# Kernel tuning notes

Measured on AMD Instinct MI355X. Metric: run time of the kernel, lower is better.

Reference implementation:

```python
import jax, jax.numpy as jnp
import numpy as np

# Dims: batch B, seq L, embed D, router hidden H, num_blocks NB, top_k K
B, L, D, H, NB, K = 8, 4096, 1024, 64, 16, 2
TEMP = 2.0          # current_temperature buffer (init 2.0), clamp(min=0.1) inert
LN_EPS = 1e-5


def setup_inputs() -> dict:
    key = jax.random.key(0)
    k_x, k_w1, k_w2 = jax.random.split(key, 3)
    return {
        "x": jax.random.normal(k_x, (B, L, D), dtype=jnp.float32),
        "ln_gamma": jnp.ones((D,), dtype=jnp.float32),
        "ln_beta": jnp.zeros((D,), dtype=jnp.float32),
        "W1": jax.random.normal(k_w1, (D, H), dtype=jnp.float32) / np.sqrt(D).astype(np.float32),
        "W2": jax.random.normal(k_w2, (H, NB), dtype=jnp.float32) / np.sqrt(H).astype(np.float32),
    }


def reference(x, ln_gamma, ln_beta, W1, W2):
    # gate: LayerNorm -> Linear(no bias) -> GELU(exact) -> Linear(no bias)
    mu = jnp.mean(x, axis=-1, keepdims=True)
    var = jnp.mean(jnp.square(x - mu), axis=-1, keepdims=True)
    xn = (x - mu) * jax.lax.rsqrt(var + LN_EPS) * ln_gamma + ln_beta
    h = jax.nn.gelu(xn @ W1, approximate=False)          # (B, L, H)
    logits = (h @ W2) / TEMP                              # (B, L, NB)

    probs = jax.nn.softmax(logits, axis=-1)               # (B, L, NB)
    top_probs, indices = jax.lax.top_k(probs, K)          # (B, L, K) each
    weights = top_probs / (jnp.sum(top_probs, axis=-1, keepdims=True) + 1e-8)

    # load-balancing aux loss: f = fraction of assignments per block (detached),
    # P = mean router prob per block
    counts = jnp.zeros((NB,), dtype=probs.dtype).at[indices.reshape(-1)].add(1.0)
    f = jax.lax.stop_gradient(counts) / (B * L * K + 1e-8)
    P = jnp.mean(probs, axis=(0, 1))                      # (NB,)
    aux_loss = NB * jnp.sum(f * P)

    return probs, indices, aux_loss, weights
```

## Files before the change

kernel.cpp:

```cpp
#include <hip/hip_runtime.h>
#include <math.h>

typedef __attribute__((ext_vector_type(8))) short short8;
typedef __attribute__((ext_vector_type(4))) float f32x4;

#define NTOK 32768
#define DDIM 1024
#define HDIM 64
#define NB 16
#define LN_EPS 1e-5f

#define IDX_OFF ((size_t)NTOK * NB)
#define AUX_OFF (IDX_OFF + (size_t)NTOK * 2)
#define WT_OFF  (AUX_OFF + 1)

#define CS_F   64
#define BP_F   4352
#define PART_F 102656

__device__ __forceinline__ short8 as_s8(uint4 u) {
    union { uint4 u; short8 s; } x; x.u = u; return x.s;
}

__device__ __forceinline__ f32x4 ntload4(const float* p) {
    return __builtin_nontemporal_load((const f32x4*)p);
}

__global__ void pack_kernel(const float* __restrict__ W1,
                            const float* __restrict__ gamma,
                            const float* __restrict__ beta,
                            float* __restrict__ ws) {
    __shared__ float sg[4][64];
    __shared__ float sb[4][64];
    const int s = blockIdx.x;
    const int t = threadIdx.x;

    {
        const int j = t & 63, p = t >> 6;
        float ag = 0.f, ab = 0.f;
        for (int kk = 0; kk < 8; ++kk) {
            const int k = s * 32 + p * 8 + kk;
            const float w = W1[k * HDIM + j];
            ag += gamma[k] * w;
            ab += beta[k] * w;
        }
        sg[p][j] = ag;
        sb[p][j] = ab;
    }

    {
        unsigned int* bp = (unsigned int*)(ws + BP_F);
        const int n = t >> 6;
        const int l = t & 63;
        const int q = l >> 4, c = l & 15;
        const int col = n * 16 + c;
        unsigned int uh[8], um[8], ul[8];
#pragma unroll
        for (int j = 0; j < 8; ++j) {
            const int k = s * 32 + q * 8 + j;
            const float w = gamma[k] * W1[k * HDIM + col];
            const unsigned int hb = __float_as_uint(w) & 0xFFFF0000u;
            const float r = w - __uint_as_float(hb);
            const unsigned int mb = __float_as_uint(r) & 0xFFFF0000u;
            const float r2 = r - __uint_as_float(mb);
            const unsigned int lb = __float_as_uint(r2) & 0xFFFF0000u;
            uh[j] = hb >> 16; um[j] = mb >> 16; ul[j] = lb >> 16;
        }
        const int base = ((s * 4 + n) * 64 + l) * 4;
#pragma unroll
        for (int d = 0; d < 4; ++d) {
            bp[base + d]         = uh[2 * d] | (uh[2 * d + 1] << 16);
            bp[32768 + base + d] = um[2 * d] | (um[2 * d + 1] << 16);
            bp[65536 + base + d] = ul[2 * d] | (ul[2 * d + 1] << 16);
        }
    }
    __syncthreads();
    if (t < 64) {
        atomicAdd(&ws[CS_F + t],      sg[0][t] + sg[1][t] + sg[2][t] + sg[3][t]);
        atomicAdd(&ws[CS_F + 64 + t], sb[0][t] + sb[1][t] + sb[2][t] + sb[3][t]);
    }
}

__device__ __forceinline__ void split8(const f32x4 a0, const f32x4 a1,
                                       short8& AH, short8& AM, short8& AL,
                                       float& s1, float& s2) {
    const float v[8] = {a0.x, a0.y, a0.z, a0.w, a1.x, a1.y, a1.z, a1.w};
    unsigned int ph[4], pm[4], pl[4];
#pragma unroll
    for (int d = 0; d < 4; ++d) {
        const float v0 = v[2 * d], v1 = v[2 * d + 1];
        const unsigned int h0 = __float_as_uint(v0) & 0xFFFF0000u;
        const unsigned int h1 = __float_as_uint(v1) & 0xFFFF0000u;
        const float r0 = v0 - __uint_as_float(h0);
        const float r1 = v1 - __uint_as_float(h1);
        const unsigned int m0 = __float_as_uint(r0) & 0xFFFF0000u;
        const unsigned int m1 = __float_as_uint(r1) & 0xFFFF0000u;
        const float q0 = r0 - __uint_as_float(m0);
        const float q1 = r1 - __uint_as_float(m1);
        ph[d] = (h0 >> 16) | h1;
        pm[d] = (m0 >> 16) | m1;
        pl[d] = (__float_as_uint(q0) >> 16) | (__float_as_uint(q1) & 0xFFFF0000u);
        s1 += v0 + v1;
        s2 = fmaf(v0, v0, fmaf(v1, v1, s2));
    }
    AH = as_s8(make_uint4(ph[0], ph[1], ph[2], ph[3]));
    AM = as_s8(make_uint4(pm[0], pm[1], pm[2], pm[3]));
    AL = as_s8(make_uint4(pl[0], pl[1], pl[2], pl[3]));
}

#define MFMA6(ACC, AH, AM, AL, BH, BM, BL)                                        \
    ACC = __builtin_amdgcn_mfma_f32_16x16x32_bf16(AH, as_s8(BH), ACC, 0, 0, 0);   \
    ACC = __builtin_amdgcn_mfma_f32_16x16x32_bf16(AH, as_s8(BM), ACC, 0, 0, 0);   \
    ACC = __builtin_amdgcn_mfma_f32_16x16x32_bf16(AM, as_s8(BH), ACC, 0, 0, 0);   \
    ACC = __builtin_amdgcn_mfma_f32_16x16x32_bf16(AH, as_s8(BL), ACC, 0, 0, 0);   \
    ACC = __builtin_amdgcn_mfma_f32_16x16x32_bf16(AM, as_s8(BM), ACC, 0, 0, 0);   \
    ACC = __builtin_amdgcn_mfma_f32_16x16x32_bf16(AL, as_s8(BH), ACC, 0, 0, 0);

__global__ __launch_bounds__(256, 2)
void router_main(const float* __restrict__ x,
                 const float* __restrict__ ws_ro,
                 const unsigned int* __restrict__ bp,
                 const float* __restrict__ W2,
                 float* __restrict__ part,
                 float* __restrict__ out) {
    __shared__ float smem[8736];
    float* ypart = smem;
    float* s1l   = smem + 8320;
    float* s2l   = smem + 8448;
    float* csgl  = smem + 8576;
    float* csbl  = smem + 8640;
    float* cntl  = smem + 8704;
    float* w2l   = smem + 4160;
    float* llds  = smem + 6240;

    const int t    = threadIdx.x;
    const int wv   = t >> 6;
    const int lane = t & 63;
    const int q = lane >> 4, c = lane & 15;
    const int g  = wv & 1;
    const int kh = wv >> 1;
    const int tok0 = blockIdx.x * 64;
    const int tokw = tok0 + g * 32;

    if (t < 64) { csgl[t] = ws_ro[CS_F + t]; csbl[t] = ws_ro[CS_F + 64 + t]; }
    if (t < 16) cntl[t] = 0.f;

    const float* xr0 = x + (size_t)(tokw + c) * DDIM + kh * 512 + q * 8;
    const float* xr1 = xr0 + (size_t)16 * DDIM;
    const unsigned int* bpl = bp + lane * 4;

    f32x4 acc0[4] = {{0.f,0.f,0.f,0.f},{0.f,0.f,0.f,0.f},{0.f,0.f,0.f,0.f},{0.f,0.f,0.f,0.f}};
    f32x4 acc1[4] = {{0.f,0.f,0.f,0.f},{0.f,0.f,0.f,0.f},{0.f,0.f,0.f,0.f},{0.f,0.f,0.f,0.f}};
    float s1a = 0.f, s2a = 0.f, s1b = 0.f, s2b = 0.f;

    f32x4 a00 = ntload4(xr0),      a01 = ntload4(xr0 + 4);
    f32x4 a10 = ntload4(xr1),      a11 = ntload4(xr1 + 4);
    f32x4 b00 = ntload4(xr0 + 32), b01 = ntload4(xr0 + 36);
    f32x4 b10 = ntload4(xr1 + 32), b11 = ntload4(xr1 + 36);

    for (int it = 0; it < 16; ++it) {
        const int s = kh * 16 + it;

        uint4 bh[4], bm[4], bl[4];
#pragma unroll
        for (int n = 0; n < 4; ++n) {
            bh[n] = *(const uint4*)(bpl + (s * 4 + n) * 256);
            bm[n] = *(const uint4*)(bpl + 32768 + (s * 4 + n) * 256);
            bl[n] = *(const uint4*)(bpl + 65536 + (s * 4 + n) * 256);
        }
        const int off = ((it + 2) & 15) * 32;
        const f32x4 p00 = ntload4(xr0 + off), p01 = ntload4(xr0 + off + 4);
        const f32x4 p10 = ntload4(xr1 + off), p11 = ntload4(xr1 + off + 4);

        short8 AH0, AM0, AL0, AH1, AM1, AL1;
        split8(a00, a01, AH0, AM0, AL0, s1a, s2a);
        split8(a10, a11, AH1, AM1, AL1, s1b, s2b);

#pragma unroll
        for (int n = 0; n < 4; ++n) {
            MFMA6(acc0[n], AH0, AM0, AL0, bh[n], bm[n], bl[n]);
            MFMA6(acc1[n], AH1, AM1, AL1, bh[n], bm[n], bl[n]);
        }
        a00 = b00; a01 = b01; a10 = b10; a11 = b11;
        b00 = p00; b01 = p01; b10 = p10; b11 = p11;
    }

    s1a += __shfl_xor(s1a, 16, 64); s1a += __shfl_xor(s1a, 32, 64);
    s2a += __shfl_xor(s2a, 16, 64); s2a += __shfl_xor(s2a, 32, 64);
    s1b += __shfl_xor(s1b, 16, 64); s1b += __shfl_xor(s1b, 32, 64);
    s2b += __shfl_xor(s2b, 16, 64); s2b += __shfl_xor(s2b, 32, 64);
    if (lane < 16) {
        s1l[wv * 32 + c] = s1a;      s2l[wv * 32 + c] = s2a;
        s1l[wv * 32 + 16 + c] = s1b; s2l[wv * 32 + 16 + c] = s2b;
    }

#pragma unroll
    for (int n = 0; n < 4; ++n)
#pragma unroll
        for (int r = 0; r < 4; ++r) {
            ypart[wv * 2080 + (q * 4 + r) * 65 + n * 16 + c]      = acc0[n][r];
            ypart[wv * 2080 + (16 + q * 4 + r) * 65 + n * 16 + c] = acc1[n][r];
        }
    __syncthreads();

    {
        const int m = t >> 2, cb = (t & 3) * 16;
        const int gg = m >> 5, lm = m & 31;
        const float S1 = s1l[gg * 32 + lm] + s1l[(2 + gg) * 32 + lm];
        const float S2 = s2l[gg * 32 + lm] + s2l[(2 + gg) * 32 + lm];
        const float mu   = S1 * (1.0f / 1024.0f);
        const float var  = S2 * (1.0f / 1024.0f) - mu * mu;
        const float rstd = 1.0f / sqrtf(var + LN_EPS);
#pragma unroll
        for (int cc = 0; cc < 16; ++cc) {
            const int col = cb + cc;
            const float y = ypart[gg * 2080 + lm * 65 + col]
                          + ypart[(2 + gg) * 2080 + lm * 65 + col];
            const float pre = rstd * (y - mu * csgl[col]) + csbl[col];
            ypart[gg * 2080 + lm * 65 + col] =
                0.5f * pre * (1.0f + erff(pre * 0.70710678118654752f));
        }
    }
    __syncthreads();

    {
        const float4 wv4 = *(const float4*)(W2 + t * 4);
        const int j = t >> 2, gq = (t & 3) * 4;
        w2l[j * 17 + gq + 0] = wv4.x; w2l[j * 17 + gq + 1] = wv4.y;
        w2l[j * 17 + gq + 2] = wv4.z; w2l[j * 17 + gq + 3] = wv4.w;
    }
    __syncthreads();

    {
        const int m2 = t >> 2, nb0 = (t & 3) * 4;
        const int g2 = m2 >> 5, lm2 = m2 & 31;
        const float* hrow = ypart + g2 * 2080 + lm2 * 65;
        float l0 = 0.f, l1 = 0.f, l2 = 0.f, l3 = 0.f;
#pragma unroll
        for (int j = 0; j < 64; ++j) {
            const float h = hrow[j];
            l0 = fmaf(h, w2l[j * 17 + nb0 + 0], l0);
            l1 = fmaf(h, w2l[j * 17 + nb0 + 1], l1);
            l2 = fmaf(h, w2l[j * 17 + nb0 + 2], l2);
            l3 = fmaf(h, w2l[j * 17 + nb0 + 3], l3);
        }
        llds[m2 * 17 + nb0 + 0] = l0 * 0.5f;
        llds[m2 * 17 + nb0 + 1] = l1 * 0.5f;
        llds[m2 * 17 + nb0 + 2] = l2 * 0.5f;
        llds[m2 * 17 + nb0 + 3] = l3 * 0.5f;
    }
    __syncthreads();

    if (t < 64) {
        float p[16];
        float mx = -1e30f;
#pragma unroll
        for (int i = 0; i < NB; ++i) { p[i] = llds[t * 17 + i]; mx = fmaxf(mx, p[i]); }
        float s = 0.f;
#pragma unroll
        for (int i = 0; i < NB; ++i) { p[i] = expf(p[i] - mx); s += p[i]; }
        const float inv = 1.0f / s;
#pragma unroll
        for (int i = 0; i < NB; ++i) { p[i] *= inv; llds[t * 17 + i] = p[i]; }

        float* po = out + (size_t)(tok0 + t) * NB;
#pragma unroll
        for (int u = 0; u < 4; ++u) {
            float4 v; v.x = p[u*4]; v.y = p[u*4+1]; v.z = p[u*4+2]; v.w = p[u*4+3];
            *(float4*)(po + u * 4) = v;
        }

        float b0 = -1.f, b1 = -1.f;
        int i0 = 0, i1 = 0;
#pragma unroll
        for (int i = 0; i < NB; ++i) {
            if (p[i] > b0)      { b1 = b0; i1 = i0; b0 = p[i]; i0 = i; }
            else if (p[i] > b1) { b1 = p[i]; i1 = i; }
        }
        const float wsum = b0 + b1 + 1e-8f;
        out[IDX_OFF + (size_t)(tok0 + t) * 2]     = (float)i0;
        out[IDX_OFF + (size_t)(tok0 + t) * 2 + 1] = (float)i1;
        out[WT_OFF + (size_t)(tok0 + t) * 2]      = b0 / wsum;
        out[WT_OFF + (size_t)(tok0 + t) * 2 + 1]  = b1 / wsum;
        atomicAdd(&cntl[i0], 1.0f);
        atomicAdd(&cntl[i1], 1.0f);
    }
    __syncthreads();

    if (t < 16) {
        float ps = 0.f;
        for (int m = 0; m < 64; ++m) ps += llds[m * 17 + t];
        part[(size_t)blockIdx.x * 32 + 16 + t] = ps;
        part[(size_t)blockIdx.x * 32 + t]      = cntl[t];
    }
}

__global__ void aux_kernel(const float* __restrict__ part,
                           float* __restrict__ gacc,
                           float* __restrict__ out) {
    __shared__ float red[8][32];
    __shared__ float flag;
    const int t = threadIdx.x;
    const int b = blockIdx.x;
    const int i = t & 31, rr = t >> 5;
    const int r0 = b * 16 + rr;
    red[rr][i] = part[(size_t)r0 * 32 + i] + part[(size_t)(r0 + 8) * 32 + i];
    __syncthreads();
    if (t < 32) {
        float tot = 0.f;
#pragma unroll
        for (int p = 0; p < 8; ++p) tot += red[p][t];
        atomicAdd(&gacc[t], tot);
    }
    __syncthreads();
    if (t == 0) {
        __threadfence();
        const unsigned int old = atomicAdd((unsigned int*)(gacc + 32), 1u);
        flag = (old == 31u) ? 1.f : 0.f;
    }
    __syncthreads();
    if (flag != 0.f) {
        if (t < 32) red[0][t] = atomicAdd(&gacc[t], 0.0f);
        __syncthreads();
        if (t == 0) {
            float a = 0.f;
            for (int k = 0; k < NB; ++k) {
                const float f = red[0][k] / (65536.0f + 1e-8f);
                const float P = red[0][16 + k] * (1.0f / 32768.0f);
                a += f * P;
            }
            out[AUX_OFF] = 16.0f * a;
        }
    }
}

extern "C" void kernel_launch(void* const* d_in, const int* in_sizes, int n_in,
                              void* d_out, int out_size, void* d_ws, size_t ws_size,
                              hipStream_t stream) {
    const float* x     = (const float*)d_in[0];
    const float* gamma = (const float*)d_in[1];
    const float* beta  = (const float*)d_in[2];
    const float* W1    = (const float*)d_in[3];
    const float* W2    = (const float*)d_in[4];
    float* out = (float*)d_out;
    float* ws  = (float*)d_ws;

    (void)hipMemsetAsync(ws, 0, 192 * sizeof(float), stream);
    pack_kernel<<<32, 256, 0, stream>>>(W1, gamma, beta, ws);
    router_main<<<NTOK / 64, 256, 0, stream>>>(x, ws, (const unsigned int*)(ws + BP_F),
                                               W2, ws + PART_F, out);
    aux_kernel<<<32, 256, 0, stream>>>(ws + PART_F, ws, out);
}
```

Baseline: 225.8 us.

## Halve tokens per block and split K across four waves for more blocks

Each router block now handles 32 tokens instead of 64, with all four waves splitting the 1024-wide reduction into quarters rather than two token groups times two halves. The grid doubles to 1024 blocks and launch bounds request four blocks per SM, giving more parallelism and occupancy. Per-block partial sums are merged by atomic adds into the existing part rows, and pack_kernel zeroes those rows first. The cost is more LDS cross-wave reduction, per-block setup and weight-fragment loads across more blocks, plus atomic contention.

```diff
diff --git a/kernel.cpp b/kernel.cpp
--- a/kernel.cpp
+++ b/kernel.cpp
@@ -34,6 +34,11 @@
     __shared__ float sb[4][64];
     const int s = blockIdx.x;
     const int t = threadIdx.x;
+
+    {
+        float* pz = ws + PART_F + ((size_t)s * 256 + t) * 2;
+        pz[0] = 0.f; pz[1] = 0.f;
+    }
 
     {
         const int j = t & 63, p = t >> 6;
@@ -116,7 +121,7 @@
     ACC = __builtin_amdgcn_mfma_f32_16x16x32_bf16(AM, as_s8(BM), ACC, 0, 0, 0);   \
     ACC = __builtin_amdgcn_mfma_f32_16x16x32_bf16(AL, as_s8(BH), ACC, 0, 0, 0);
 
-__global__ __launch_bounds__(256, 2)
+__global__ __launch_bounds__(256, 4)
 void router_main(const float* __restrict__ x,
                  const float* __restrict__ ws_ro,
                  const unsigned int* __restrict__ bp,
@@ -137,15 +142,13 @@
     const int wv   = t >> 6;
     const int lane = t & 63;
     const int q = lane >> 4, c = lane & 15;
-    const int g  = wv & 1;
-    const int kh = wv >> 1;
-    const int tok0 = blockIdx.x * 64;
-    const int tokw = tok0 + g * 32;
+    const int kh = wv;
+    const int tok0 = blockIdx.x * 32;
 
     if (t < 64) { csgl[t] = ws_ro[CS_F + t]; csbl[t] = ws_ro[CS_F + 64 + t]; }
     if (t < 16) cntl[t] = 0.f;
 
-    const float* xr0 = x + (size_t)(tokw + c) * DDIM + kh * 512 + q * 8;
+    const float* xr0 = x + (size_t)(tok0 + c) * DDIM + kh * 256 + q * 8;
     const float* xr1 = xr0 + (size_t)16 * DDIM;
     const unsigned int* bpl = bp + lane * 4;
 
@@ -158,8 +161,8 @@
     f32x4 b00 = ntload4(xr0 + 32), b01 = ntload4(xr0 + 36);
     f32x4 b10 = ntload4(xr1 + 32), b11 = ntload4(xr1 + 36);
 
-    for (int it = 0; it < 16; ++it) {
-        const int s = kh * 16 + it;
+    for (int it = 0; it < 8; ++it) {
+        const int s = kh * 8 + it;
 
         uint4 bh[4], bm[4], bl[4];
 #pragma unroll
@@ -168,7 +171,7 @@
             bm[n] = *(const uint4*)(bpl + 32768 + (s * 4 + n) * 256);
             bl[n] = *(const uint4*)(bpl + 65536 + (s * 4 + n) * 256);
         }
-        const int off = ((it + 2) & 15) * 32;
+        const int off = ((it + 2) & 7) * 32;
         const f32x4 p00 = ntload4(xr0 + off), p01 = ntload4(xr0 + off + 4);
         const f32x4 p10 = ntload4(xr1 + off), p11 = ntload4(xr1 + off + 4);
 
@@ -204,20 +207,21 @@
     __syncthreads();
 
     {
-        const int m = t >> 2, cb = (t & 3) * 16;
-        const int gg = m >> 5, lm = m & 31;
-        const float S1 = s1l[gg * 32 + lm] + s1l[(2 + gg) * 32 + lm];
-        const float S2 = s2l[gg * 32 + lm] + s2l[(2 + gg) * 32 + lm];
+        const int m = t >> 3, cb = (t & 7) * 8;
+        const float S1 = s1l[m] + s1l[32 + m] + s1l[64 + m] + s1l[96 + m];
+        const float S2 = s2l[m] + s2l[32 + m] + s2l[64 + m] + s2l[96 + m];
         const float mu   = S1 * (1.0f / 1024.0f);
         const float var  = S2 * (1.0f / 1024.0f) - mu * mu;
         const float rstd = 1.0f / sqrtf(var + LN_EPS);
 #pragma unroll
-        for (int cc = 0; cc < 16; ++cc) {
+        for (int cc = 0; cc < 8; ++cc) {
             const int col = cb + cc;
-            const float y = ypart[gg * 2080 + lm * 65 + col]
-                          + ypart[(2 + gg) * 2080 + lm * 65 + col];
+            const float y = ypart[m * 65 + col]
+                          + ypart[2080 + m * 65 + col]
+                          + ypart[4160 + m * 65 + col]
+                          + ypart[6240 + m * 65 + col];
             const float pre = rstd * (y - mu * csgl[col]) + csbl[col];
-            ypart[gg * 2080 + lm * 65 + col] =
+            ypart[m * 65 + col] =
                 0.5f * pre * (1.0f + erff(pre * 0.70710678118654752f));
         }
     }
@@ -232,26 +236,21 @@
     __syncthreads();
 
     {
-        const int m2 = t >> 2, nb0 = (t & 3) * 4;
-        const int g2 = m2 >> 5, lm2 = m2 & 31;
-        const float* hrow = ypart + g2 * 2080 + lm2 * 65;
-        float l0 = 0.f, l1 = 0.f, l2 = 0.f, l3 = 0.f;
+        const int m2 = t >> 3, nb0 = (t & 7) * 2;
+        const float* hrow = ypart + m2 * 65;
+        float l0 = 0.f, l1 = 0.f;
 #pragma unroll
         for (int j = 0; j < 64; ++j) {
             const float h = hrow[j];
             l0 = fmaf(h, w2l[j * 17 + nb0 + 0], l0);
             l1 = fmaf(h, w2l[j * 17 + nb0 + 1], l1);
-            l2 = fmaf(h, w2l[j * 17 + nb0 + 2], l2);
-            l3 = fmaf(h, w2l[j * 17 + nb0 + 3], l3);
         }
         llds[m2 * 17 + nb0 + 0] = l0 * 0.5f;
         llds[m2 * 17 + nb0 + 1] = l1 * 0.5f;
-        llds[m2 * 17 + nb0 + 2] = l2 * 0.5f;
-        llds[m2 * 17 + nb0 + 3] = l3 * 0.5f;
-    }
-    __syncthreads();
-
-    if (t < 64) {
+    }
+    __syncthreads();
+
+    if (t < 32) {
         float p[16];
         float mx = -1e30f;
 #pragma unroll
@@ -289,9 +288,10 @@
 
     if (t < 16) {
         float ps = 0.f;
-        for (int m = 0; m < 64; ++m) ps += llds[m * 17 + t];
-        part[(size_t)blockIdx.x * 32 + 16 + t] = ps;
-        part[(size_t)blockIdx.x * 32 + t]      = cntl[t];
+        for (int m = 0; m < 32; ++m) ps += llds[m * 17 + t];
+        const size_t row = (size_t)(blockIdx.x >> 1) * 32;
+        atomicAdd(&part[row + 16 + t], ps);
+        atomicAdd(&part[row + t], cntl[t]);
     }
 }
 
@@ -347,7 +347,7 @@
 
     (void)hipMemsetAsync(ws, 0, 192 * sizeof(float), stream);
     pack_kernel<<<32, 256, 0, stream>>>(W1, gamma, beta, ws);
-    router_main<<<NTOK / 64, 256, 0, stream>>>(x, ws, (const unsigned int*)(ws + BP_F),
+    router_main<<<NTOK / 32, 256, 0, stream>>>(x, ws, (const unsigned int*)(ws + BP_F),
                                                W2, ws + PART_F, out);
     aux_kernel<<<32, 256, 0, stream>>>(ws + PART_F, ws, out);
 }
```

Result: slower. 241.3 us (+6.8%).

## Stage packed W1 in LDS with double buffering and give each wave full K

Applied to the files above, without the earlier changes.

Each block now covers 128 tokens, and each wave owns 32 tokens across the full 1024-wide reduction. This removes the split-K partial-sum exchange through shared memory. The packed bf16 W1 slices are staged cooperatively into double-buffered LDS per K-step, replacing per-wave global loads of the same weights, at the cost of a __syncthreads every step. LayerNorm stats and GELU are applied directly from the accumulator registers via shuffles, and the second GEMV is vectorized. The block count is halved, which may reduce occupancy and latency hiding; the aux kernel grid and its completion counter are adjusted to match.

```diff
diff --git a/kernel.cpp b/kernel.cpp
--- a/kernel.cpp
+++ b/kernel.cpp
@@ -116,6 +116,39 @@
     ACC = __builtin_amdgcn_mfma_f32_16x16x32_bf16(AM, as_s8(BM), ACC, 0, 0, 0);   \
     ACC = __builtin_amdgcn_mfma_f32_16x16x32_bf16(AL, as_s8(BH), ACC, 0, 0, 0);
 
+#define STEP(S, CUR, NXT, DOSTAGE)                                               \
+    {                                                                            \
+        const int off = (((S) + 2) & 31) * 32;                                   \
+        const f32x4 p00 = ntload4(xr0 + off), p01 = ntload4(xr0 + off + 4);      \
+        const f32x4 p10 = ntload4(xr1 + off), p11 = ntload4(xr1 + off + 4);      \
+        uint4 st0, st1, st2;                                                     \
+        if (DOSTAGE) {                                                           \
+            const unsigned int* sp = bp + ((S) + 1) * 1024 + t * 4;              \
+            st0 = *(const uint4*)(sp);                                           \
+            st1 = *(const uint4*)(sp + 32768);                                   \
+            st2 = *(const uint4*)(sp + 65536);                                   \
+        }                                                                        \
+        short8 AH0, AM0, AL0, AH1, AM1, AL1;                                     \
+        split8(a00, a01, AH0, AM0, AL0, s1a, s2a);                               \
+        split8(a10, a11, AH1, AM1, AL1, s1b, s2b);                               \
+        _Pragma("unroll")                                                        \
+        for (int n = 0; n < 4; ++n) {                                            \
+            const uint4 bh = *(const uint4*)((CUR) + n * 256 + lane * 4);        \
+            const uint4 bm = *(const uint4*)((CUR) + 1024 + n * 256 + lane * 4); \
+            const uint4 bl = *(const uint4*)((CUR) + 2048 + n * 256 + lane * 4); \
+            MFMA6(acc0[n], AH0, AM0, AL0, bh, bm, bl);                           \
+            MFMA6(acc1[n], AH1, AM1, AL1, bh, bm, bl);                           \
+        }                                                                        \
+        a00 = b00; a01 = b01; a10 = b10; a11 = b11;                              \
+        b00 = p00; b01 = p01; b10 = p10; b11 = p11;                              \
+        if (DOSTAGE) {                                                           \
+            *(uint4*)((NXT) + t * 4)        = st0;                               \
+            *(uint4*)((NXT) + 1024 + t * 4) = st1;                               \
+            *(uint4*)((NXT) + 2048 + t * 4) = st2;                               \
+        }                                                                        \
+        __syncthreads();                                                         \
+    }
+
 __global__ __launch_bounds__(256, 2)
 void router_main(const float* __restrict__ x,
                  const float* __restrict__ ws_ro,
@@ -123,31 +156,40 @@
                  const float* __restrict__ W2,
                  float* __restrict__ part,
                  float* __restrict__ out) {
-    __shared__ float smem[8736];
-    float* ypart = smem;
-    float* s1l   = smem + 8320;
-    float* s2l   = smem + 8448;
-    float* csgl  = smem + 8576;
-    float* csbl  = smem + 8640;
-    float* cntl  = smem + 8704;
-    float* w2l   = smem + 4160;
-    float* llds  = smem + 6240;
+    __shared__ __align__(16) float smem[14480];
+    float* bstage = smem;
+    float* hlds   = smem + 6144;
+    float* cntl   = smem + 14464;
+    float* w2l    = smem;
+    float* llds   = smem + 1024;
 
     const int t    = threadIdx.x;
     const int wv   = t >> 6;
     const int lane = t & 63;
     const int q = lane >> 4, c = lane & 15;
-    const int g  = wv & 1;
-    const int kh = wv >> 1;
-    const int tok0 = blockIdx.x * 64;
-    const int tokw = tok0 + g * 32;
-
-    if (t < 64) { csgl[t] = ws_ro[CS_F + t]; csbl[t] = ws_ro[CS_F + 64 + t]; }
+    const int tok0 = blockIdx.x * 128;
+    const int tokw = tok0 + wv * 32;
+
     if (t < 16) cntl[t] = 0.f;
 
-    const float* xr0 = x + (size_t)(tokw + c) * DDIM + kh * 512 + q * 8;
+    float csg[4], csb[4];
+#pragma unroll
+    for (int n = 0; n < 4; ++n) {
+        csg[n] = ws_ro[CS_F + n * 16 + c];
+        csb[n] = ws_ro[CS_F + 64 + n * 16 + c];
+    }
+
+    const float* xr0 = x + (size_t)(tokw + c) * DDIM + q * 8;
     const float* xr1 = xr0 + (size_t)16 * DDIM;
-    const unsigned int* bpl = bp + lane * 4;
+
+    {
+        uint4 s0 = *(const uint4*)(bp + t * 4);
+        uint4 s1 = *(const uint4*)(bp + 32768 + t * 4);
+        uint4 s2 = *(const uint4*)(bp + 65536 + t * 4);
+        *(uint4*)(bstage + t * 4)        = s0;
+        *(uint4*)(bstage + 1024 + t * 4) = s1;
+        *(uint4*)(bstage + 2048 + t * 4) = s2;
+    }
 
     f32x4 acc0[4] = {{0.f,0.f,0.f,0.f},{0.f,0.f,0.f,0.f},{0.f,0.f,0.f,0.f},{0.f,0.f,0.f,0.f}};
     f32x4 acc1[4] = {{0.f,0.f,0.f,0.f},{0.f,0.f,0.f,0.f},{0.f,0.f,0.f,0.f},{0.f,0.f,0.f,0.f}};
@@ -158,110 +200,74 @@
     f32x4 b00 = ntload4(xr0 + 32), b01 = ntload4(xr0 + 36);
     f32x4 b10 = ntload4(xr1 + 32), b11 = ntload4(xr1 + 36);
 
-    for (int it = 0; it < 16; ++it) {
-        const int s = kh * 16 + it;
-
-        uint4 bh[4], bm[4], bl[4];
-#pragma unroll
-        for (int n = 0; n < 4; ++n) {
-            bh[n] = *(const uint4*)(bpl + (s * 4 + n) * 256);
-            bm[n] = *(const uint4*)(bpl + 32768 + (s * 4 + n) * 256);
-            bl[n] = *(const uint4*)(bpl + 65536 + (s * 4 + n) * 256);
-        }
-        const int off = ((it + 2) & 15) * 32;
-        const f32x4 p00 = ntload4(xr0 + off), p01 = ntload4(xr0 + off + 4);
-        const f32x4 p10 = ntload4(xr1 + off), p11 = ntload4(xr1 + off + 4);
-
-        short8 AH0, AM0, AL0, AH1, AM1, AL1;
-        split8(a00, a01, AH0, AM0, AL0, s1a, s2a);
-        split8(a10, a11, AH1, AM1, AL1, s1b, s2b);
-
-#pragma unroll
-        for (int n = 0; n < 4; ++n) {
-            MFMA6(acc0[n], AH0, AM0, AL0, bh[n], bm[n], bl[n]);
-            MFMA6(acc1[n], AH1, AM1, AL1, bh[n], bm[n], bl[n]);
-        }
-        a00 = b00; a01 = b01; a10 = b10; a11 = b11;
-        b00 = p00; b01 = p01; b10 = p10; b11 = p11;
+    __syncthreads();
+
+    float* const bufA = bstage;
+    float* const bufB = bstage + 3072;
+#pragma unroll 1
+    for (int s2i = 0; s2i < 16; ++s2i) {
+        const int s = s2i * 2;
+        STEP(s,     bufA, bufB, 1)
+        STEP(s + 1, bufB, bufA, (s2i < 15))
     }
 
     s1a += __shfl_xor(s1a, 16, 64); s1a += __shfl_xor(s1a, 32, 64);
     s2a += __shfl_xor(s2a, 16, 64); s2a += __shfl_xor(s2a, 32, 64);
     s1b += __shfl_xor(s1b, 16, 64); s1b += __shfl_xor(s1b, 32, 64);
     s2b += __shfl_xor(s2b, 16, 64); s2b += __shfl_xor(s2b, 32, 64);
-    if (lane < 16) {
-        s1l[wv * 32 + c] = s1a;      s2l[wv * 32 + c] = s2a;
-        s1l[wv * 32 + 16 + c] = s1b; s2l[wv * 32 + 16 + c] = s2b;
-    }
-
-#pragma unroll
-    for (int n = 0; n < 4; ++n)
+
+    *(float4*)(w2l + t * 4) = *(const float4*)(W2 + t * 4);
+
+    {
+        float* hw = hlds + wv * 2080;
 #pragma unroll
         for (int r = 0; r < 4; ++r) {
-            ypart[wv * 2080 + (q * 4 + r) * 65 + n * 16 + c]      = acc0[n][r];
-            ypart[wv * 2080 + (16 + q * 4 + r) * 65 + n * 16 + c] = acc1[n][r];
-        }
-    __syncthreads();
-
-    {
-        const int m = t >> 2, cb = (t & 3) * 16;
-        const int gg = m >> 5, lm = m & 31;
-        const float S1 = s1l[gg * 32 + lm] + s1l[(2 + gg) * 32 + lm];
-        const float S2 = s2l[gg * 32 + lm] + s2l[(2 + gg) * 32 + lm];
-        const float mu   = S1 * (1.0f / 1024.0f);
-        const float var  = S2 * (1.0f / 1024.0f) - mu * mu;
-        const float rstd = 1.0f / sqrtf(var + LN_EPS);
-#pragma unroll
-        for (int cc = 0; cc < 16; ++cc) {
-            const int col = cb + cc;
-            const float y = ypart[gg * 2080 + lm * 65 + col]
-                          + ypart[(2 + gg) * 2080 + lm * 65 + col];
-            const float pre = rstd * (y - mu * csgl[col]) + csbl[col];
-            ypart[gg * 2080 + lm * 65 + col] =
-                0.5f * pre * (1.0f + erff(pre * 0.70710678118654752f));
-        }
-    }
-    __syncthreads();
-
-    {
-        const float4 wv4 = *(const float4*)(W2 + t * 4);
-        const int j = t >> 2, gq = (t & 3) * 4;
-        w2l[j * 17 + gq + 0] = wv4.x; w2l[j * 17 + gq + 1] = wv4.y;
-        w2l[j * 17 + gq + 2] = wv4.z; w2l[j * 17 + gq + 3] = wv4.w;
-    }
-    __syncthreads();
-
-    {
-        const int m2 = t >> 2, nb0 = (t & 3) * 4;
-        const int g2 = m2 >> 5, lm2 = m2 & 31;
-        const float* hrow = ypart + g2 * 2080 + lm2 * 65;
-        float l0 = 0.f, l1 = 0.f, l2 = 0.f, l3 = 0.f;
-#pragma unroll
+            const int tt = q * 4 + r;
+            const float S1A = __shfl(s1a, tt, 64), S2A = __shfl(s2a, tt, 64);
+            const float S1B = __shfl(s1b, tt, 64), S2B = __shfl(s2b, tt, 64);
+            const float muA = S1A * (1.0f / 1024.0f);
+            const float rsA = 1.0f / sqrtf(S2A * (1.0f / 1024.0f) - muA * muA + LN_EPS);
+            const float muB = S1B * (1.0f / 1024.0f);
+            const float rsB = 1.0f / sqrtf(S2B * (1.0f / 1024.0f) - muB * muB + LN_EPS);
+#pragma unroll
+            for (int n = 0; n < 4; ++n) {
+                const float preA = rsA * (acc0[n][r] - muA * csg[n]) + csb[n];
+                const float preB = rsB * (acc1[n][r] - muB * csg[n]) + csb[n];
+                hw[tt * 65 + n * 16 + c] =
+                    0.5f * preA * (1.0f + erff(preA * 0.70710678118654752f));
+                hw[(16 + tt) * 65 + n * 16 + c] =
+                    0.5f * preB * (1.0f + erff(preB * 0.70710678118654752f));
+            }
+        }
+    }
+    __syncthreads();
+
+    {
+        const int m2 = t >> 1, o = (t & 1) * 8;
+        const float* hrow = hlds + (m2 >> 5) * 2080 + (m2 & 31) * 65;
+        f32x4 L0 = {0.f, 0.f, 0.f, 0.f}, L1 = {0.f, 0.f, 0.f, 0.f};
+#pragma unroll 8
         for (int j = 0; j < 64; ++j) {
             const float h = hrow[j];
-            l0 = fmaf(h, w2l[j * 17 + nb0 + 0], l0);
-            l1 = fmaf(h, w2l[j * 17 + nb0 + 1], l1);
-            l2 = fmaf(h, w2l[j * 17 + nb0 + 2], l2);
-            l3 = fmaf(h, w2l[j * 17 + nb0 + 3], l3);
-        }
-        llds[m2 * 17 + nb0 + 0] = l0 * 0.5f;
-        llds[m2 * 17 + nb0 + 1] = l1 * 0.5f;
-        llds[m2 * 17 + nb0 + 2] = l2 * 0.5f;
-        llds[m2 * 17 + nb0 + 3] = l3 * 0.5f;
-    }
-    __syncthreads();
-
-    if (t < 64) {
+            L0 += *(const f32x4*)(w2l + j * 16 + o) * h;
+            L1 += *(const f32x4*)(w2l + j * 16 + o + 4) * h;
+        }
+        *(f32x4*)(llds + m2 * 16 + o)     = L0 * 0.5f;
+        *(f32x4*)(llds + m2 * 16 + o + 4) = L1 * 0.5f;
+    }
+    __syncthreads();
+
+    if (t < 128) {
         float p[16];
         float mx = -1e30f;
 #pragma unroll
-        for (int i = 0; i < NB; ++i) { p[i] = llds[t * 17 + i]; mx = fmaxf(mx, p[i]); }
-        float s = 0.f;
-#pragma unroll
-        for (int i = 0; i < NB; ++i) { p[i] = expf(p[i] - mx); s += p[i]; }
-        const float inv = 1.0f / s;
-#pragma unroll
-        for (int i = 0; i < NB; ++i) { p[i] *= inv; llds[t * 17 + i] = p[i]; }
+        for (int i = 0; i < NB; ++i) { p[i] = llds[t * 16 + i]; mx = fmaxf(mx, p[i]); }
+        float ssum = 0.f;
+#pragma unroll
+        for (int i = 0; i < NB; ++i) { p[i] = expf(p[i] - mx); ssum += p[i]; }
+        const float inv = 1.0f / ssum;
+#pragma unroll
+        for (int i = 0; i < NB; ++i) { p[i] *= inv; llds[t * 16 + i] = p[i]; }
 
         float* po = out + (size_t)(tok0 + t) * NB;
 #pragma unroll
@@ -289,9 +295,9 @@
 
     if (t < 16) {
         float ps = 0.f;
-        for (int m = 0; m < 64; ++m) ps += llds[m * 17 + t];
+        for (int m = 0; m < 128; ++m) ps += llds[m * 16 + t];
+        part[(size_t)blockIdx.x * 32 + t]      = cntl[t];
         part[(size_t)blockIdx.x * 32 + 16 + t] = ps;
-        part[(size_t)blockIdx.x * 32 + t]      = cntl[t];
     }
 }
 
@@ -316,7 +322,7 @@
     if (t == 0) {
         __threadfence();
         const unsigned int old = atomicAdd((unsigned int*)(gacc + 32), 1u);
-        flag = (old == 31u) ? 1.f : 0.f;
+        flag = (old == 15u) ? 1.f : 0.f;
     }
     __syncthreads();
     if (flag != 0.f) {
@@ -347,7 +353,7 @@
 
     (void)hipMemsetAsync(ws, 0, 192 * sizeof(float), stream);
     pack_kernel<<<32, 256, 0, stream>>>(W1, gamma, beta, ws);
-    router_main<<<NTOK / 64, 256, 0, stream>>>(x, ws, (const unsigned int*)(ws + BP_F),
-                                               W2, ws + PART_F, out);
-    aux_kernel<<<32, 256, 0, stream>>>(ws + PART_F, ws, out);
-}
+    router_main<<<NTOK / 128, 256, 0, stream>>>(x, ws, (const unsigned int*)(ws + BP_F),
+                                                W2, ws + PART_F, out);
+    aux_kernel<<<16, 256, 0, stream>>>(ws + PART_F, ws, out);
+}
```

New measurement: 230.0 us. Within noise of the previous version (+1.9%).
